# Performance work log

Measured on AMD Instinct MI355X. Metric: run time of the kernel, lower is better.

The kernel has to match this reference:

```python
import jax, jax.numpy as jnp
import numpy as np

B, T, C, H = 4, 2048, 1024, 16
HD = C // H  # head_dim = 64


def setup_inputs() -> dict:
    key = jax.random.key(0)
    k1, k2, k3, k4, k5 = jax.random.split(key, 5)
    s = 1.0 / np.sqrt(C)
    return {
        "x": jax.random.normal(k1, (B, T, C), dtype=jnp.float32),
        "Wqkv": jax.random.normal(k2, (C, 3 * C), dtype=jnp.float32) * s,
        "bqkv": jnp.zeros((3 * C,), dtype=jnp.float32),
        "Wproj": jax.random.normal(k3, (C, C), dtype=jnp.float32) * s,
        "bproj": jnp.zeros((C,), dtype=jnp.float32),
    }


def reference(x, Wqkv, bqkv, Wproj, bproj):
    b, t, c = x.shape
    qkv = x @ Wqkv + bqkv                      # [B,T,3C]
    q, k, v = jnp.split(qkv, 3, axis=-1)
    # [B,T,C] -> [B,H,T,HD]
    q = q.reshape(b, t, H, HD).transpose(0, 2, 1, 3)
    k = k.reshape(b, t, H, HD).transpose(0, 2, 1, 3)
    v = v.reshape(b, t, H, HD).transpose(0, 2, 1, 3)
    att = jnp.einsum("bhqd,bhkd->bhqk", q, k) * (1.0 / np.sqrt(HD))
    causal = jnp.tril(jnp.ones((t, t), dtype=bool))
    att = jnp.where(causal[None, None], att, -jnp.inf)
    att = jax.nn.softmax(att, axis=-1)
    # dropout p=0.0 (eval) -> identity
    y = jnp.einsum("bhqk,bhkd->bhqd", att, v)  # [B,H,T,HD]
    y = y.transpose(0, 2, 1, 3).reshape(b, t, c)
    return y @ Wproj + bproj
```

## Files before the change

kernel.cpp:

```cpp
#include <hip/hip_runtime.h>


typedef unsigned short u16;
typedef short short8_t __attribute__((ext_vector_type(8)));
typedef float f32x4 __attribute__((ext_vector_type(4)));

#define B_ 4
#define T_ 2048
#define C_ 1024
#define H_ 16
#define HD_ 64
#define QSCALE 0.18033688011112042f

__device__ __forceinline__ u16 f32_to_bf16(float f) {
  unsigned int u = __float_as_uint(f);
  u += 0x7fffu + ((u >> 16) & 1u);
  return (u16)(u >> 16);
}

__device__ __forceinline__ void async_copy16(const void* g, void* l) {
  __builtin_amdgcn_global_load_lds((const __attribute__((address_space(1))) void*)g,
                                   (__attribute__((address_space(3))) void*)l, 16, 0, 0);
}

__device__ __forceinline__ void transpose_tile(const float* __restrict__ in,
                                               u16* __restrict__ out, int K, int N, int bx, int by,
                                               float (*tile)[33], int tid) {
  int nb = bx * 32, kb = by * 32;
  int c = tid & 31, r0 = tid >> 5;
#pragma unroll
  for (int rr = 0; rr < 4; ++rr) {
    int r = r0 + rr * 8;
    tile[r][c] = in[(size_t)(kb + r) * N + nb + c];
  }
  __syncthreads();
#pragma unroll
  for (int rr = 0; rr < 4; ++rr) {
    int r = r0 + rr * 8;
    out[(size_t)(nb + r) * K + kb + c] = f32_to_bf16(tile[c][r]);
  }
}

__global__ void prep_kernel(const float* __restrict__ x, u16* __restrict__ Xb,
                            const float* __restrict__ Wqkv, u16* __restrict__ WqkvT,
                            const float* __restrict__ Wproj, u16* __restrict__ WprojT) {
  __shared__ float tile[32][33];
  int id = blockIdx.x;
  int tid = threadIdx.x;
  if (id < 8192) {
    int i = id * 256 + tid;
    float4 v = ((const float4*)x)[i];
    unsigned int a = (unsigned int)f32_to_bf16(v.x) | ((unsigned int)f32_to_bf16(v.y) << 16);
    unsigned int b = (unsigned int)f32_to_bf16(v.z) | ((unsigned int)f32_to_bf16(v.w) << 16);
    ((uint2*)Xb)[i] = make_uint2(a, b);
  } else if (id < 11264) {
    int t = id - 8192;
    transpose_tile(Wqkv, WqkvT, C_, 3 * C_, t % 96, t / 96, tile, tid);
  } else {
    int t = id - 11264;
    transpose_tile(Wproj, WprojT, C_, C_, t % 32, t / 32, tile, tid);
  }
}

__device__ __forceinline__ void stage_tile(const u16* __restrict__ A, const u16* __restrict__ Bt,
                                           int K, int m0, int n0, int k0, char* buf, int tid) {
#pragma unroll
  for (int it = 0; it < 2; ++it) {
    int j = it * 256 + tid;
    int row = j >> 2;
    int ch = ((j & 3) ^ (row >> 1)) & 3;
    async_copy16(A + (size_t)(m0 + row) * K + k0 + ch * 8, buf + j * 16);
    async_copy16(Bt + (size_t)(n0 + row) * K + k0 + ch * 8, buf + 8192 + j * 16);
  }
}

__device__ __forceinline__ void gemm_mainloop(const u16* __restrict__ A, const u16* __restrict__ Bt,
                                              int K, int m0, int n0, char* smem,
                                              f32x4 (&acc)[4][4]) {
  int tid = threadIdx.x;
  int lane = tid & 63, wave = tid >> 6;
  int quad = lane >> 4, l15 = lane & 15;
  int waveM = wave >> 1, waveN = wave & 1;
  stage_tile(A, Bt, K, m0, n0, 0, smem, tid);
  int nIter = K >> 5;
  for (int ki = 0; ki < nIter; ++ki) {
    int cur = ki & 1;
    char* bufc = smem + cur * 16384;
    __syncthreads();
    if (ki + 1 < nIter)
      stage_tile(A, Bt, K, m0, n0, (ki + 1) << 5, smem + (cur ^ 1) * 16384, tid);
    short8_t af[4], bfr[4];
#pragma unroll
    for (int mt = 0; mt < 4; ++mt) {
      int row = waveM * 64 + mt * 16 + l15;
      af[mt] = *(const short8_t*)(bufc + row * 64 + (((quad ^ (row >> 1)) & 3) << 4));
    }
#pragma unroll
    for (int nt = 0; nt < 4; ++nt) {
      int row = waveN * 64 + nt * 16 + l15;
      bfr[nt] = *(const short8_t*)(bufc + 8192 + row * 64 + (((quad ^ (row >> 1)) & 3) << 4));
    }
#pragma unroll
    for (int mt = 0; mt < 4; ++mt)
#pragma unroll
      for (int nt = 0; nt < 4; ++nt)
        acc[mt][nt] = __builtin_amdgcn_mfma_f32_16x16x32_bf16(af[mt], bfr[nt], acc[mt][nt], 0, 0, 0);
  }
}

__global__ __launch_bounds__(256, 2) void gemm1_kernel(const u16* __restrict__ A,
                                                       const u16* __restrict__ Bt,
                                                       const float* __restrict__ bias,
                                                       u16* __restrict__ Qo, u16* __restrict__ Ko,
                                                       u16* __restrict__ Vo) {
  __shared__ __align__(128) char smem[32768];
  f32x4 acc[4][4];
#pragma unroll
  for (int mt = 0; mt < 4; ++mt)
#pragma unroll
    for (int nt = 0; nt < 4; ++nt) acc[mt][nt] = (f32x4){0.f, 0.f, 0.f, 0.f};
  int m0 = blockIdx.y * 128, n0 = blockIdx.x * 128;
  gemm_mainloop(A, Bt, C_, m0, n0, smem, acc);

  int lane = threadIdx.x & 63, wave = threadIdx.x >> 6;
  int quad = lane >> 4, l15 = lane & 15;
  int waveM = wave >> 1, waveN = wave & 1;

  if (n0 < 2048) {
#pragma unroll
    for (int nt = 0; nt < 4; ++nt) {
      int n = n0 + waveN * 64 + nt * 16;
      int which = n >> 10;
      int rem = n & 1023;
      int head = rem >> 6;
      int d = (rem & 63) + l15;
      float bv = bias[n + l15];
      float sc = (which == 0) ? QSCALE : 1.0f;
      u16* dst = (which == 0) ? Qo : Ko;
#pragma unroll
      for (int mt = 0; mt < 4; ++mt) {
#pragma unroll
        for (int r = 0; r < 4; ++r) {
          int token = m0 + waveM * 64 + mt * 16 + quad * 4 + r;
          int b = token >> 11, t = token & 2047;
          dst[(((size_t)(b * H_ + head)) * T_ + t) * HD_ + d] =
              f32_to_bf16((acc[mt][nt][r] + bv) * sc);
        }
      }
    }
  } else {
    __syncthreads();
    char* W = smem + wave * 8192;
#pragma unroll
    for (int nt = 0; nt < 4; ++nt) {
      int nl = nt * 16 + l15;
      float bv = bias[n0 + waveN * 64 + nl];
#pragma unroll
      for (int mt = 0; mt < 4; ++mt) {
        int g = mt * 4 + quad;
        int pc = ((g >> 1) ^ (nl & 7)) & 7;
        uint2 pv;
        pv.x = (unsigned int)f32_to_bf16(acc[mt][nt][0] + bv) |
               ((unsigned int)f32_to_bf16(acc[mt][nt][1] + bv) << 16);
        pv.y = (unsigned int)f32_to_bf16(acc[mt][nt][2] + bv) |
               ((unsigned int)f32_to_bf16(acc[mt][nt][3] + bv) << 16);
        *(uint2*)(W + nl * 128 + pc * 16 + (g & 1) * 8) = pv;
      }
    }
    int b = m0 >> 11;
#pragma unroll
    for (int i = 0; i < 8; ++i) {
      int jj = i * 64 + lane;
      int nl = jj >> 3;
      int c = jj & 7;
      int pc = c ^ (nl & 7);
      uint4 v = *(const uint4*)(W + nl * 128 + pc * 16);
      int rem = (n0 - 2048) + waveN * 64 + nl;
      int head = rem >> 6, dd = rem & 63;
      int t0 = (m0 & 2047) + waveM * 64 + c * 8;
      *(uint4*)(Vo + ((size_t)(b * H_ + head) * HD_ + dd) * T_ + t0) = v;
    }
  }
}

__global__ __launch_bounds__(256, 2) void gemm2_kernel(const u16* __restrict__ A,
                                                       const u16* __restrict__ Bt,
                                                       const float* __restrict__ bias,
                                                       float* __restrict__ out) {
  __shared__ __align__(128) char smem[32768];
  f32x4 acc[4][4];
#pragma unroll
  for (int mt = 0; mt < 4; ++mt)
#pragma unroll
    for (int nt = 0; nt < 4; ++nt) acc[mt][nt] = (f32x4){0.f, 0.f, 0.f, 0.f};
  int m0 = blockIdx.y * 128, n0 = blockIdx.x * 128;
  gemm_mainloop(A, Bt, C_, m0, n0, smem, acc);

  int lane = threadIdx.x & 63, wave = threadIdx.x >> 6;
  int quad = lane >> 4, l15 = lane & 15;
  int waveM = wave >> 1, waveN = wave & 1;
#pragma unroll
  for (int nt = 0; nt < 4; ++nt) {
    int col = n0 + waveN * 64 + nt * 16 + l15;
    float bv = bias[col];
#pragma unroll
    for (int mt = 0; mt < 4; ++mt) {
#pragma unroll
      for (int r = 0; r < 4; ++r) {
        int token = m0 + waveM * 64 + mt * 16 + quad * 4 + r;
        out[(size_t)token * C_ + col] = acc[mt][nt][r] + bv;
      }
    }
  }
}

__device__ __forceinline__ void stage_kv(const u16* __restrict__ Kb, const u16* __restrict__ Vb,
                                         int kt, char* Ksb, char* Vsb, int tid) {
#pragma unroll
  for (int it = 0; it < 2; ++it) {
    int j = it * 256 + tid;
    int row = j >> 3;
    int ch = (j & 7) ^ (row & 7);
    async_copy16(Kb + (size_t)(kt * 64 + row) * HD_ + ch * 8, Ksb + j * 16);
    async_copy16(Vb + (size_t)row * T_ + kt * 64 + ch * 8, Vsb + j * 16);
  }
}

__global__ __launch_bounds__(256, 3) void attn_kernel(const u16* __restrict__ Qg,
                                                      const u16* __restrict__ Kg,
                                                      const u16* __restrict__ Vg,
                                                      u16* __restrict__ Yg) {
  __shared__ __align__(128) char smem[49152];
  int tid = threadIdx.x;
  int wave = tid >> 6, lane = tid & 63;
  int quad = lane >> 4, l15 = lane & 15;
  char* Psw = smem + 32768 + wave * 4096;
  int bh = blockIdx.x;
  int qt = 15 - blockIdx.y;
  int b = bh >> 4, h = bh & 15;
  const u16* Kb = Kg + (size_t)bh * T_ * HD_;
  const u16* Vb = Vg + (size_t)bh * HD_ * T_;

  short8_t qf[2][2];
#pragma unroll
  for (int mt = 0; mt < 2; ++mt)
#pragma unroll
    for (int ks = 0; ks < 2; ++ks) {
      int row = qt * 128 + wave * 32 + mt * 16 + l15;
      qf[mt][ks] = *(const short8_t*)(Qg + ((size_t)bh * T_ + row) * HD_ + ks * 32 + quad * 8);
    }

  stage_kv(Kb, Vb, 0, smem, smem + 16384, tid);

  float l_part[2][4];
  f32x4 o[2][4];
#pragma unroll
  for (int mt = 0; mt < 2; ++mt)
#pragma unroll
    for (int r = 0; r < 4; ++r) l_part[mt][r] = 0.f;
#pragma unroll
  for (int mt = 0; mt < 2; ++mt)
#pragma unroll
    for (int dt = 0; dt < 4; ++dt) o[mt][dt] = (f32x4){0.f, 0.f, 0.f, 0.f};

  int ktmax_blk = 2 * qt + 1;
  int ktmax_wave = 2 * qt + (wave >> 1);
  for (int kt = 0; kt <= ktmax_blk; ++kt) {
    int cur = kt & 1;
    char* Ksc = smem + cur * 8192;
    char* Vtc = smem + 16384 + cur * 8192;
    __syncthreads();
    if (kt < ktmax_blk)
      stage_kv(Kb, Vb, kt + 1, smem + (cur ^ 1) * 8192, smem + 16384 + (cur ^ 1) * 8192, tid);
    if (kt > ktmax_wave) continue;

    f32x4 s[2][4];
#pragma unroll
    for (int mt = 0; mt < 2; ++mt)
#pragma unroll
      for (int nt = 0; nt < 4; ++nt) s[mt][nt] = (f32x4){0.f, 0.f, 0.f, 0.f};
#pragma unroll
    for (int ks = 0; ks < 2; ++ks) {
      short8_t bfr[4];
#pragma unroll
      for (int nt = 0; nt < 4; ++nt) {
        int row = nt * 16 + l15;
        bfr[nt] = *(const short8_t*)(Ksc + row * 128 + ((((ks * 4 + quad) ^ row) & 7) << 4));
      }
#pragma unroll
      for (int mt = 0; mt < 2; ++mt)
#pragma unroll
        for (int nt = 0; nt < 4; ++nt)
          s[mt][nt] =
              __builtin_amdgcn_mfma_f32_16x16x32_bf16(qf[mt][ks], bfr[nt], s[mt][nt], 0, 0, 0);
    }

    if (kt == ktmax_wave) {
#pragma unroll
      for (int mt = 0; mt < 2; ++mt) {
        int qrow0 = qt * 128 + wave * 32 + mt * 16 + quad * 4;
#pragma unroll
        for (int nt = 0; nt < 4; ++nt) {
          int col = kt * 64 + nt * 16 + l15;
#pragma unroll
          for (int r = 0; r < 4; ++r) {
            float p = __builtin_amdgcn_exp2f(s[mt][nt][r]);
            if (col > qrow0 + r) p = 0.f;
            s[mt][nt][r] = p;
          }
        }
      }
    } else {
#pragma unroll
      for (int mt = 0; mt < 2; ++mt)
#pragma unroll
        for (int nt = 0; nt < 4; ++nt)
#pragma unroll
          for (int r = 0; r < 4; ++r) s[mt][nt][r] = __builtin_amdgcn_exp2f(s[mt][nt][r]);
    }

#pragma unroll
    for (int mt = 0; mt < 2; ++mt) {
#pragma unroll
      for (int r = 0; r < 4; ++r)
        l_part[mt][r] += (s[mt][0][r] + s[mt][1][r]) + (s[mt][2][r] + s[mt][3][r]);
#pragma unroll
      for (int nt = 0; nt < 4; ++nt) {
        int col = nt * 16 + l15;
#pragma unroll
        for (int r = 0; r < 4; ++r) {
          int prow = mt * 16 + quad * 4 + r;
          *(u16*)(Psw + prow * 128 + ((((col >> 3) ^ prow) & 7) << 4) + ((col & 7) << 1)) =
              (u16)(__float_as_uint(s[mt][nt][r]) >> 16);
        }
      }
    }

#pragma unroll
    for (int ks = 0; ks < 2; ++ks) {
      short8_t af[2], bfr[4];
#pragma unroll
      for (int mt = 0; mt < 2; ++mt) {
        int row = mt * 16 + l15;
        af[mt] = *(const short8_t*)(Psw + row * 128 + ((((ks * 4 + quad) ^ row) & 7) << 4));
      }
#pragma unroll
      for (int dt = 0; dt < 4; ++dt) {
        int row = dt * 16 + l15;
        bfr[dt] = *(const short8_t*)(Vtc + row * 128 + ((((ks * 4 + quad) ^ row) & 7) << 4));
      }
#pragma unroll
      for (int mt = 0; mt < 2; ++mt)
#pragma unroll
        for (int dt = 0; dt < 4; ++dt)
          o[mt][dt] = __builtin_amdgcn_mfma_f32_16x16x32_bf16(af[mt], bfr[dt], o[mt][dt], 0, 0, 0);
    }
  }

#pragma unroll
  for (int mt = 0; mt < 2; ++mt) {
#pragma unroll
    for (int r = 0; r < 4; ++r) {
      float lsum = l_part[mt][r];
#pragma unroll
      for (int off = 1; off < 16; off <<= 1) lsum += __shfl_xor(lsum, off);
      float inv = 1.0f / lsum;
#pragma unroll
      for (int dt = 0; dt < 4; ++dt) {
        int t = qt * 128 + wave * 32 + mt * 16 + quad * 4 + r;
        float val = o[mt][dt][r] * inv;
        Yg[((size_t)(b * T_ + t)) * C_ + h * HD_ + dt * 16 + l15] = f32_to_bf16(val);
      }
    }
  }
}

extern "C" void kernel_launch(void* const* d_in, const int* in_sizes, int n_in,
                              void* d_out, int out_size, void* d_ws, size_t ws_size,
                              hipStream_t stream) {
  (void)in_sizes; (void)n_in; (void)out_size; (void)ws_size;
  const float* x = (const float*)d_in[0];
  const float* Wqkv = (const float*)d_in[1];
  const float* bqkv = (const float*)d_in[2];
  const float* Wproj = (const float*)d_in[3];
  const float* bproj = (const float*)d_in[4];
  float* out = (float*)d_out;
  char* ws = (char*)d_ws;

  u16* Xb = (u16*)ws;
  u16* WqkvT = (u16*)(ws + 16777216);
  u16* WprojT = (u16*)(ws + 16777216 + 6291456);
  u16* Q = (u16*)(ws + 25165824);
  u16* K = Q + 8388608;
  u16* V = K + 8388608;
  u16* Y = Xb;

  prep_kernel<<<12288, 256, 0, stream>>>(x, Xb, Wqkv, WqkvT, Wproj, WprojT);
  gemm1_kernel<<<dim3(24, 64), 256, 0, stream>>>(Xb, WqkvT, bqkv, Q, K, V);
  attn_kernel<<<dim3(64, 16), 256, 0, stream>>>(Q, K, V, Y);
  gemm2_kernel<<<dim3(8, 64), 256, 0, stream>>>(Y, WprojT, bproj, out);
}
```

Baseline: 239.6 us.

## Rewrite QKV GEMM with 256x256 tiles and 4-stage async LDS pipeline

Replaces the 128x128, 256-thread QKV projection GEMM with a 256x256 tile, 512-thread kernel that prefetches three k-slices ahead into a 4-buffer LDS ring. It uses explicit vmcnt waits, raw s_barrier and setprio around MFMA bursts. Staging of the A and B halves of the next slice is interleaved with compute. The aim is more data reuse per tile and better hiding of global-load latency. In exchange it uses 128KB of LDS per block (one block per CU) and launches fewer blocks, which risks tail imbalance.

After: 253.8 us. 5.9% more time.

```diff
diff --git a/kernel.cpp b/kernel.cpp
--- a/kernel.cpp
+++ b/kernel.cpp
@@ -21,6 +21,12 @@
 __device__ __forceinline__ void async_copy16(const void* g, void* l) {
   __builtin_amdgcn_global_load_lds((const __attribute__((address_space(1))) void*)g,
                                    (__attribute__((address_space(3))) void*)l, 16, 0, 0);
+}
+
+__device__ __forceinline__ void wave_barrier() { asm volatile("s_barrier" ::: "memory"); }
+template <int N>
+__device__ __forceinline__ void wait_vmcnt() {
+  asm volatile("s_waitcnt vmcnt(%0)" ::"i"(N) : "memory");
 }
 
 __device__ __forceinline__ void transpose_tile(const float* __restrict__ in,
@@ -62,6 +68,155 @@
   }
 }
 
+__device__ __forceinline__ void g1_stageA(const u16* __restrict__ A, char* dst, int m0, int kt,
+                                          int tid) {
+  int row = tid >> 2;
+  int c = (tid & 3) ^ (row & 3);
+  const u16* src = A + (size_t)(m0 + row) * C_ + kt * 32 + c * 8;
+  async_copy16(src, dst + tid * 16);
+  async_copy16(src + (size_t)128 * C_, dst + 8192 + tid * 16);
+}
+__device__ __forceinline__ void g1_stageB(const u16* __restrict__ Bt, char* dst, int n0, int kt,
+                                          int tid) {
+  int row = tid >> 2;
+  int c = (tid & 3) ^ (row & 3);
+  const u16* src = Bt + (size_t)(n0 + row) * C_ + kt * 32 + c * 8;
+  async_copy16(src, dst + 16384 + tid * 16);
+  async_copy16(src + (size_t)128 * C_, dst + 24576 + tid * 16);
+}
+
+template <bool STAGE, int W>
+__device__ __forceinline__ void g1_group(const u16* __restrict__ A, const u16* __restrict__ Bt,
+                                         char* smem, int m0, int n0, int g, int tid, int aoff,
+                                         int boff, f32x4 (&acc)[8][4]) {
+  if (STAGE) g1_stageA(A, smem + ((g + 3) & 3) * 32768, m0, g + 3, tid);
+  wait_vmcnt<W>();
+  wave_barrier();
+  char* base = smem + (g & 3) * 32768;
+  short8_t af[4], bf[4];
+#pragma unroll
+  for (int i = 0; i < 4; ++i) af[i] = *(const short8_t*)(base + aoff + i * 1024);
+#pragma unroll
+  for (int i = 0; i < 4; ++i) bf[i] = *(const short8_t*)(base + boff + i * 1024);
+  __builtin_amdgcn_s_setprio(1);
+#pragma unroll
+  for (int mt = 0; mt < 4; ++mt)
+#pragma unroll
+    for (int nt = 0; nt < 4; ++nt)
+      acc[mt][nt] = __builtin_amdgcn_mfma_f32_16x16x32_bf16(af[mt], bf[nt], acc[mt][nt], 0, 0, 0);
+  __builtin_amdgcn_s_setprio(0);
+  if (STAGE) g1_stageB(Bt, smem + ((g + 3) & 3) * 32768, n0, g + 3, tid);
+#pragma unroll
+  for (int i = 0; i < 4; ++i) af[i] = *(const short8_t*)(base + aoff + 4096 + i * 1024);
+  __builtin_amdgcn_s_setprio(1);
+#pragma unroll
+  for (int mt = 0; mt < 4; ++mt)
+#pragma unroll
+    for (int nt = 0; nt < 4; ++nt)
+      acc[4 + mt][nt] =
+          __builtin_amdgcn_mfma_f32_16x16x32_bf16(af[mt], bf[nt], acc[4 + mt][nt], 0, 0, 0);
+  __builtin_amdgcn_s_setprio(0);
+  wave_barrier();
+}
+
+__global__ __launch_bounds__(512, 2) void gemm1_kernel(const u16* __restrict__ A,
+                                                       const u16* __restrict__ Bt,
+                                                       const float* __restrict__ bias,
+                                                       u16* __restrict__ Qo, u16* __restrict__ Ko,
+                                                       u16* __restrict__ Vo) {
+  __shared__ __align__(128) char smem[131072];
+  int tid = threadIdx.x;
+  int lane = tid & 63, wave = tid >> 6;
+  int quad = lane >> 4, l15 = lane & 15;
+  int waveM = wave >> 2, waveN = wave & 3;
+  int m0 = blockIdx.y * 256, n0 = blockIdx.x * 256;
+
+  f32x4 acc[8][4];
+#pragma unroll
+  for (int mt = 0; mt < 8; ++mt)
+#pragma unroll
+    for (int nt = 0; nt < 4; ++nt) acc[mt][nt] = (f32x4){0.f, 0.f, 0.f, 0.f};
+
+  int swz = (quad ^ (l15 & 3)) << 4;
+  int aoff = waveM * 8192 + l15 * 64 + swz;
+  int boff = 16384 + (waveN >> 1) * 8192 + (waveN & 1) * 4096 + l15 * 64 + swz;
+
+  g1_stageA(A, smem, m0, 0, tid);
+  g1_stageB(Bt, smem, n0, 0, tid);
+  g1_stageA(A, smem + 32768, m0, 1, tid);
+  g1_stageB(Bt, smem + 32768, n0, 1, tid);
+  g1_stageA(A, smem + 65536, m0, 2, tid);
+  g1_stageB(Bt, smem + 65536, n0, 2, tid);
+  wait_vmcnt<8>();
+  wave_barrier();
+
+#pragma unroll 4
+  for (int g = 0; g < 29; ++g) g1_group<true, 10>(A, Bt, smem, m0, n0, g, tid, aoff, boff, acc);
+  g1_group<false, 8>(A, Bt, smem, m0, n0, 29, tid, aoff, boff, acc);
+  g1_group<false, 4>(A, Bt, smem, m0, n0, 30, tid, aoff, boff, acc);
+  g1_group<false, 0>(A, Bt, smem, m0, n0, 31, tid, aoff, boff, acc);
+
+  int nb = n0 + waveN * 64;
+  if (n0 < 2048) {
+#pragma unroll
+    for (int nt = 0; nt < 4; ++nt) {
+      int n = nb + nt * 16;
+      int which = n >> 10;
+      int rem = n & 1023;
+      int head = rem >> 6;
+      int d = (rem & 63) + l15;
+      float bv = bias[n + l15];
+      float sc = (which == 0) ? QSCALE : 1.0f;
+      u16* dst = (which == 0) ? Qo : Ko;
+#pragma unroll
+      for (int mt = 0; mt < 8; ++mt) {
+#pragma unroll
+        for (int r = 0; r < 4; ++r) {
+          int token = m0 + waveM * 128 + mt * 16 + quad * 4 + r;
+          int b = token >> 11, t = token & 2047;
+          dst[(((size_t)(b * H_ + head)) * T_ + t) * HD_ + d] =
+              f32_to_bf16((acc[mt][nt][r] + bv) * sc);
+        }
+      }
+    }
+  } else {
+    char* W = smem + wave * 8192;
+    int b = m0 >> 11;
+#pragma unroll
+    for (int mh = 0; mh < 2; ++mh) {
+#pragma unroll
+      for (int nt = 0; nt < 4; ++nt) {
+        int nl = nt * 16 + l15;
+        float bv = bias[nb + nl];
+#pragma unroll
+        for (int mtp = 0; mtp < 4; ++mtp) {
+          int mt = mh * 4 + mtp;
+          int g = mtp * 4 + quad;
+          int pc = ((g >> 1) ^ (nl & 7)) & 7;
+          uint2 pv;
+          pv.x = (unsigned int)f32_to_bf16(acc[mt][nt][0] + bv) |
+                 ((unsigned int)f32_to_bf16(acc[mt][nt][1] + bv) << 16);
+          pv.y = (unsigned int)f32_to_bf16(acc[mt][nt][2] + bv) |
+                 ((unsigned int)f32_to_bf16(acc[mt][nt][3] + bv) << 16);
+          *(uint2*)(W + nl * 128 + pc * 16 + (g & 1) * 8) = pv;
+        }
+      }
+#pragma unroll
+      for (int i = 0; i < 8; ++i) {
+        int jj = i * 64 + lane;
+        int nl = jj >> 3;
+        int c = jj & 7;
+        int pc = c ^ (nl & 7);
+        uint4 v = *(const uint4*)(W + nl * 128 + pc * 16);
+        int rem = (nb - 2048) + nl;
+        int head = rem >> 6, dd = rem & 63;
+        int t0 = (m0 & 2047) + waveM * 128 + mh * 64 + c * 8;
+        *(uint4*)(Vo + ((size_t)(b * H_ + head) * HD_ + dd) * T_ + t0) = v;
+      }
+    }
+  }
+}
+
 __device__ __forceinline__ void stage_tile(const u16* __restrict__ A, const u16* __restrict__ Bt,
                                            int K, int m0, int n0, int k0, char* buf, int tid) {
 #pragma unroll
@@ -108,81 +263,6 @@
   }
 }
 
-__global__ __launch_bounds__(256, 2) void gemm1_kernel(const u16* __restrict__ A,
-                                                       const u16* __restrict__ Bt,
-                                                       const float* __restrict__ bias,
-                                                       u16* __restrict__ Qo, u16* __restrict__ Ko,
-                                                       u16* __restrict__ Vo) {
-  __shared__ __align__(128) char smem[32768];
-  f32x4 acc[4][4];
-#pragma unroll
-  for (int mt = 0; mt < 4; ++mt)
-#pragma unroll
-    for (int nt = 0; nt < 4; ++nt) acc[mt][nt] = (f32x4){0.f, 0.f, 0.f, 0.f};
-  int m0 = blockIdx.y * 128, n0 = blockIdx.x * 128;
-  gemm_mainloop(A, Bt, C_, m0, n0, smem, acc);
-
-  int lane = threadIdx.x & 63, wave = threadIdx.x >> 6;
-  int quad = lane >> 4, l15 = lane & 15;
-  int waveM = wave >> 1, waveN = wave & 1;
-
-  if (n0 < 2048) {
-#pragma unroll
-    for (int nt = 0; nt < 4; ++nt) {
-      int n = n0 + waveN * 64 + nt * 16;
-      int which = n >> 10;
-      int rem = n & 1023;
-      int head = rem >> 6;
-      int d = (rem & 63) + l15;
-      float bv = bias[n + l15];
-      float sc = (which == 0) ? QSCALE : 1.0f;
-      u16* dst = (which == 0) ? Qo : Ko;
-#pragma unroll
-      for (int mt = 0; mt < 4; ++mt) {
-#pragma unroll
-        for (int r = 0; r < 4; ++r) {
-          int token = m0 + waveM * 64 + mt * 16 + quad * 4 + r;
-          int b = token >> 11, t = token & 2047;
-          dst[(((size_t)(b * H_ + head)) * T_ + t) * HD_ + d] =
-              f32_to_bf16((acc[mt][nt][r] + bv) * sc);
-        }
-      }
-    }
-  } else {
-    __syncthreads();
-    char* W = smem + wave * 8192;
-#pragma unroll
-    for (int nt = 0; nt < 4; ++nt) {
-      int nl = nt * 16 + l15;
-      float bv = bias[n0 + waveN * 64 + nl];
-#pragma unroll
-      for (int mt = 0; mt < 4; ++mt) {
-        int g = mt * 4 + quad;
-        int pc = ((g >> 1) ^ (nl & 7)) & 7;
-        uint2 pv;
-        pv.x = (unsigned int)f32_to_bf16(acc[mt][nt][0] + bv) |
-               ((unsigned int)f32_to_bf16(acc[mt][nt][1] + bv) << 16);
-        pv.y = (unsigned int)f32_to_bf16(acc[mt][nt][2] + bv) |
-               ((unsigned int)f32_to_bf16(acc[mt][nt][3] + bv) << 16);
-        *(uint2*)(W + nl * 128 + pc * 16 + (g & 1) * 8) = pv;
-      }
-    }
-    int b = m0 >> 11;
-#pragma unroll
-    for (int i = 0; i < 8; ++i) {
-      int jj = i * 64 + lane;
-      int nl = jj >> 3;
-      int c = jj & 7;
-      int pc = c ^ (nl & 7);
-      uint4 v = *(const uint4*)(W + nl * 128 + pc * 16);
-      int rem = (n0 - 2048) + waveN * 64 + nl;
-      int head = rem >> 6, dd = rem & 63;
-      int t0 = (m0 & 2047) + waveM * 64 + c * 8;
-      *(uint4*)(Vo + ((size_t)(b * H_ + head) * HD_ + dd) * T_ + t0) = v;
-    }
-  }
-}
-
 __global__ __launch_bounds__(256, 2) void gemm2_kernel(const u16* __restrict__ A,
                                                        const u16* __restrict__ Bt,
                                                        const float* __restrict__ bias,
@@ -396,7 +476,7 @@
   u16* Y = Xb;
 
   prep_kernel<<<12288, 256, 0, stream>>>(x, Xb, Wqkv, WqkvT, Wproj, WprojT);
-  gemm1_kernel<<<dim3(24, 64), 256, 0, stream>>>(Xb, WqkvT, bqkv, Q, K, V);
+  gemm1_kernel<<<dim3(12, 32), 512, 0, stream>>>(Xb, WqkvT, bqkv, Q, K, V);
   attn_kernel<<<dim3(64, 16), 256, 0, stream>>>(Q, K, V, Y);
   gemm2_kernel<<<dim3(8, 64), 256, 0, stream>>>(Y, WprojT, bproj, out);
 }
```
